# Optimization experiments

Measured on AMD Instinct MI355X. Metric: run time of the kernel, lower is better.

Reference implementation:

```python
import jax, jax.numpy as jnp
import numpy as np

N = 100000   # nodes
E = 1600000  # edges
IN = 32      # in_dim
D = 64       # embed_dim
G = 128      # num graphs
EPS = 1e-5   # BatchNorm eps


def setup_inputs() -> dict:
    key = jax.random.key(0)
    ks = jax.random.split(key, 12)
    s_in = 1.0 / np.sqrt(IN)
    s_d = 1.0 / np.sqrt(D)
    return {
        "x": jax.random.normal(ks[0], (N, IN), jnp.float32),
        "edge_index": jax.random.randint(ks[1], (2, E), 0, N),
        "batch": jnp.sort(jax.random.randint(ks[2], (N,), 0, G)),
        "W_embed": jax.random.normal(ks[3], (IN, D), jnp.float32) * s_in,
        "W1": jax.random.normal(ks[4], (D, D), jnp.float32) * s_d,
        "b1": jnp.zeros((D,), jnp.float32),
        "g1": jnp.ones((D,), jnp.float32),
        "bt1": jnp.zeros((D,), jnp.float32),
        "W2": jax.random.normal(ks[5], (D, D), jnp.float32) * s_d,
        "b2": jnp.zeros((D,), jnp.float32),
        "g2": jnp.ones((D,), jnp.float32),
        "bt2": jnp.zeros((D,), jnp.float32),
    }


def reference(x, edge_index, batch, W_embed, W1, b1, g1, bt1, W2, b2, g2, bt2):
    src, dst = edge_index[0], edge_index[1]
    # GCN symmetric norm with self loops: deg = in-degree + 1 (self loop)
    deg = jnp.zeros((N,), x.dtype).at[dst].add(1.0) + 1.0
    dis = jax.lax.rsqrt(deg)                      # deg^{-1/2}, [N]
    enorm = dis[src] * dis[dst]                   # per-edge norm, [E]
    self_norm = dis * dis                         # self-loop norm, [N]

    def gcn_bn(h, W, b, g, bt, relu):
        hw = h @ W                                # linear first (GCNConv)
        msg = hw[src] * enorm[:, None]            # [E, D] gather + scale
        agg = jax.ops.segment_sum(msg, dst, num_segments=N)
        agg = agg + hw * self_norm[:, None] + b   # self loops + bias
        # BatchNorm1d (training mode: batch stats, biased var)
        mu = agg.mean(axis=0)
        var = agg.var(axis=0)
        hn = (agg - mu) * jax.lax.rsqrt(var + EPS) * g + bt
        return jnp.maximum(hn, 0.0) if relu else hn

    h = x @ W_embed                               # node_embed (Linear, no bias)
    h = gcn_bn(h, W1, b1, g1, bt1, relu=True)     # ReLU only between layers
    h = gcn_bn(h, W2, b2, g2, bt2, relu=False)
    h_pool = jax.ops.segment_sum(h, batch, num_segments=G)  # global_add_pool
    return (h, h_pool)
```

## Files before the change

kernel.cpp:

```cpp
#include <hip/hip_runtime.h>

#define NN 100000
#define NE 1600000
#define IN_DIM 32
#define DD 64
#define NG 128
#define BN_EPS 1e-5f
#define AGG_BLOCKS 2048

typedef unsigned short ushort_t;
typedef unsigned int uint_t;

__device__ __forceinline__ ushort_t f2bf(float f) {
    uint_t u = __float_as_uint(f);
    u = (u + 0x7FFFu + ((u >> 16) & 1u)) >> 16;
    return (ushort_t)u;
}
__device__ __forceinline__ uint_t pack2(float a, float b) {
    return (uint_t)f2bf(a) | ((uint_t)f2bf(b) << 16);
}
__device__ __forceinline__ float bflo(uint_t u) { return __uint_as_float(u << 16); }
__device__ __forceinline__ float bfhi(uint_t u) { return __uint_as_float(u & 0xFFFF0000u); }

__global__ void init_k(int* __restrict__ ints, long n_ints, float* __restrict__ pool,
                       float* __restrict__ sums) {
    long i = (long)blockIdx.x * blockDim.x + threadIdx.x;
    if (i < n_ints) ints[i] = 0;
    if (i < (long)NG * DD) pool[i] = 0.f;
    if (i < 256) sums[i] = 0.f;
}

__global__ void deg_rank(const int* __restrict__ dst, int* __restrict__ cnt,
                         int* __restrict__ rank) {
    int e = blockIdx.x * blockDim.x + threadIdx.x;
    if (e < NE) rank[e] = atomicAdd(&cnt[dst[e]], 1);
}

__global__ __launch_bounds__(256) void alloc_k(const int* __restrict__ cnt,
                                               int* __restrict__ start,
                                               int* __restrict__ cursor,
                                               float* __restrict__ dis) {
    __shared__ int ls[256];
    __shared__ int base_s;
    int t = threadIdx.x;
    long n = (long)blockIdx.x * 256 + t;
    int v = (n < NN) ? cnt[n] : 0;
    ls[t] = v;
    __syncthreads();
    for (int off = 1; off < 256; off <<= 1) {
        int y = (t >= off) ? ls[t - off] : 0;
        __syncthreads();
        ls[t] += y;
        __syncthreads();
    }
    if (t == 0) base_s = atomicAdd(cursor, ls[255]);
    __syncthreads();
    if (n < NN) {
        start[n] = base_s + ls[t] - v;
        dis[n] = rsqrtf((float)v + 1.0f);
    }
}

__global__ void fill_edges(const int* __restrict__ src, const int* __restrict__ dstp,
                           const int* __restrict__ rank, const float* __restrict__ dis,
                           const int* __restrict__ start, uint_t* __restrict__ ep) {
    int e = blockIdx.x * blockDim.x + threadIdx.x;
    if (e >= NE) return;
    int s = src[e], t = dstp[e];
    float nm = dis[s] * dis[t];
    uint_t nb = (__float_as_uint(nm) + 0x8000u) >> 16;
    ep[start[t] + rank[e]] = (uint_t)s | ((nb & 0x7FFFu) << 17);
}

__global__ __launch_bounds__(256) void mm1_k(const float* __restrict__ x,
                                             const float* __restrict__ We,
                                             const float* __restrict__ W1,
                                             ushort_t* __restrict__ hwb) {
    __shared__ float W1s[DD * DD];
    __shared__ float Ws[IN_DIM * DD];
    int t = threadIdx.x;
    for (int i = t; i < DD * DD; i += 256) W1s[i] = W1[i];
    __syncthreads();
    for (int idx = t; idx < IN_DIM * DD; idx += 256) {
        int i = idx >> 6, j = idx & 63;
        float s = 0.f;
#pragma unroll
        for (int k = 0; k < DD; ++k) s += We[i * DD + k] * W1s[k * DD + j];
        Ws[idx] = s;
    }
    __syncthreads();
    long n = (long)blockIdx.x * 256 + t;
    if (n >= NN) return;
    float acc[DD];
#pragma unroll
    for (int d = 0; d < DD; ++d) acc[d] = 0.f;
    const float4* xr = (const float4*)(x + n * IN_DIM);
#pragma unroll
    for (int k4 = 0; k4 < IN_DIM / 4; ++k4) {
        float4 xv = xr[k4];
        const float* xp = (const float*)&xv;
#pragma unroll
        for (int kk = 0; kk < 4; ++kk) {
            float v = xp[kk];
            const float4* w4 = (const float4*)&Ws[(k4 * 4 + kk) * DD];
#pragma unroll
            for (int d4 = 0; d4 < DD / 4; ++d4) {
                float4 wv = w4[d4];
                acc[4 * d4 + 0] += v * wv.x;
                acc[4 * d4 + 1] += v * wv.y;
                acc[4 * d4 + 2] += v * wv.z;
                acc[4 * d4 + 3] += v * wv.w;
            }
        }
    }
    uint4* o = (uint4*)(hwb + n * DD);
#pragma unroll
    for (int d8 = 0; d8 < DD / 8; ++d8) {
        uint4 pk;
        pk.x = pack2(acc[8 * d8 + 0], acc[8 * d8 + 1]);
        pk.y = pack2(acc[8 * d8 + 2], acc[8 * d8 + 3]);
        pk.z = pack2(acc[8 * d8 + 4], acc[8 * d8 + 5]);
        pk.w = pack2(acc[8 * d8 + 6], acc[8 * d8 + 7]);
        o[d8] = pk;
    }
}

__global__ __launch_bounds__(256) void mm2_bn_k(const ushort_t* __restrict__ aggb,
                                                const float* __restrict__ sums,
                                                const float* __restrict__ g,
                                                const float* __restrict__ bt,
                                                const float* __restrict__ W,
                                                ushort_t* __restrict__ hwb) {
    __shared__ float Ws[DD * DD];
    __shared__ float mu_s[DD], sc_s[DD], bt_s[DD];
    int t = threadIdx.x;
    for (int i = t; i < DD * DD; i += 256) Ws[i] = W[i];
    if (t < DD) {
        const float inv_n = 1.0f / (float)NN;
        float mu = sums[t] * inv_n;
        float var = sums[64 + t] * inv_n - mu * mu;
        mu_s[t] = mu;
        sc_s[t] = g[t] * rsqrtf(var + BN_EPS);
        bt_s[t] = bt[t];
    }
    __syncthreads();
    long n = (long)blockIdx.x * 256 + t;
    if (n >= NN) return;
    float acc[DD];
#pragma unroll
    for (int d = 0; d < DD; ++d) acc[d] = 0.f;
    const uint4* ar = (const uint4*)(aggb + n * DD);
#pragma unroll
    for (int k8 = 0; k8 < DD / 8; ++k8) {
        uint4 av = ar[k8];
        float hv[8];
        hv[0] = bflo(av.x); hv[1] = bfhi(av.x);
        hv[2] = bflo(av.y); hv[3] = bfhi(av.y);
        hv[4] = bflo(av.z); hv[5] = bfhi(av.z);
        hv[6] = bflo(av.w); hv[7] = bfhi(av.w);
#pragma unroll
        for (int kk = 0; kk < 8; ++kk) {
            int k = k8 * 8 + kk;
            float h = fmaxf((hv[kk] - mu_s[k]) * sc_s[k] + bt_s[k], 0.f);
            const float4* w4 = (const float4*)&Ws[k * DD];
#pragma unroll
            for (int d4 = 0; d4 < DD / 4; ++d4) {
                float4 wv = w4[d4];
                acc[4 * d4 + 0] += h * wv.x;
                acc[4 * d4 + 1] += h * wv.y;
                acc[4 * d4 + 2] += h * wv.z;
                acc[4 * d4 + 3] += h * wv.w;
            }
        }
    }
    uint4* o = (uint4*)(hwb + n * DD);
#pragma unroll
    for (int d8 = 0; d8 < DD / 8; ++d8) {
        uint4 pk;
        pk.x = pack2(acc[8 * d8 + 0], acc[8 * d8 + 1]);
        pk.y = pack2(acc[8 * d8 + 2], acc[8 * d8 + 3]);
        pk.z = pack2(acc[8 * d8 + 4], acc[8 * d8 + 5]);
        pk.w = pack2(acc[8 * d8 + 6], acc[8 * d8 + 7]);
        o[d8] = pk;
    }
}

template <int WAGG_BF16>
__global__ __launch_bounds__(256) void gcn_agg(const ushort_t* __restrict__ hwb,
                                               const float* __restrict__ dis,
                                               const int* __restrict__ cnt,
                                               const int* __restrict__ start,
                                               const uint_t* __restrict__ ep,
                                               const float* __restrict__ bias,
                                               void* __restrict__ aggv,
                                               float* __restrict__ sums) {
    int t = threadIdx.x;
    int w = t >> 6;
    int lane = t & 63;
    int j = lane >> 3;
    int c = lane & 7;
    float selfmask = (j == 0) ? 1.f : 0.f;

    __shared__ float ls[4][128];
    for (int k = t; k < 512; k += 256) ((float*)ls)[k] = 0.f;
    __syncthreads();

    float bs[8];
#pragma unroll
    for (int k = 0; k < 8; ++k) bs[k] = bias[8 * c + k];

    for (long n = (long)blockIdx.x * 4 + w; n < NN; n += (long)gridDim.x * 4) {
        int rs = start[n];
        int ce = cnt[n];
        float sn = dis[n];
        float sq = sn * sn;

        uint4 sv = ((const uint4*)(hwb + (long)n * DD))[c];
        float acc[8];
        acc[0] = selfmask * (bflo(sv.x) * sq + bs[0]);
        acc[1] = selfmask * (bfhi(sv.x) * sq + bs[1]);
        acc[2] = selfmask * (bflo(sv.y) * sq + bs[2]);
        acc[3] = selfmask * (bfhi(sv.y) * sq + bs[3]);
        acc[4] = selfmask * (bflo(sv.z) * sq + bs[4]);
        acc[5] = selfmask * (bfhi(sv.z) * sq + bs[5]);
        acc[6] = selfmask * (bflo(sv.w) * sq + bs[6]);
        acc[7] = selfmask * (bfhi(sv.w) * sq + bs[7]);

        for (int i = 0; i < ce; i += 32) {
            int i0 = i + j, i1 = i + 8 + j, i2 = i + 16 + j, i3 = i + 24 + j;
            uint_t u0 = (i0 < ce) ? ep[rs + i0] : 0u;
            uint_t u1 = (i1 < ce) ? ep[rs + i1] : 0u;
            uint_t u2 = (i2 < ce) ? ep[rs + i2] : 0u;
            uint_t u3 = (i3 < ce) ? ep[rs + i3] : 0u;
            uint4 q0 = ((const uint4*)(hwb + (long)(u0 & 0x1FFFF) * DD))[c];
            uint4 q1 = ((const uint4*)(hwb + (long)(u1 & 0x1FFFF) * DD))[c];
            uint4 q2 = ((const uint4*)(hwb + (long)(u2 & 0x1FFFF) * DD))[c];
            uint4 q3 = ((const uint4*)(hwb + (long)(u3 & 0x1FFFF) * DD))[c];
            float n0 = __uint_as_float((u0 >> 17) << 16);
            float n1 = __uint_as_float((u1 >> 17) << 16);
            float n2 = __uint_as_float((u2 >> 17) << 16);
            float n3 = __uint_as_float((u3 >> 17) << 16);
            acc[0] += bflo(q0.x) * n0; acc[1] += bfhi(q0.x) * n0;
            acc[2] += bflo(q0.y) * n0; acc[3] += bfhi(q0.y) * n0;
            acc[4] += bflo(q0.z) * n0; acc[5] += bfhi(q0.z) * n0;
            acc[6] += bflo(q0.w) * n0; acc[7] += bfhi(q0.w) * n0;
            acc[0] += bflo(q1.x) * n1; acc[1] += bfhi(q1.x) * n1;
            acc[2] += bflo(q1.y) * n1; acc[3] += bfhi(q1.y) * n1;
            acc[4] += bflo(q1.z) * n1; acc[5] += bfhi(q1.z) * n1;
            acc[6] += bflo(q1.w) * n1; acc[7] += bfhi(q1.w) * n1;
            acc[0] += bflo(q2.x) * n2; acc[1] += bfhi(q2.x) * n2;
            acc[2] += bflo(q2.y) * n2; acc[3] += bfhi(q2.y) * n2;
            acc[4] += bflo(q2.z) * n2; acc[5] += bfhi(q2.z) * n2;
            acc[6] += bflo(q2.w) * n2; acc[7] += bfhi(q2.w) * n2;
            acc[0] += bflo(q3.x) * n3; acc[1] += bfhi(q3.x) * n3;
            acc[2] += bflo(q3.y) * n3; acc[3] += bfhi(q3.y) * n3;
            acc[4] += bflo(q3.z) * n3; acc[5] += bfhi(q3.z) * n3;
            acc[6] += bflo(q3.w) * n3; acc[7] += bfhi(q3.w) * n3;
        }

#pragma unroll
        for (int m = 8; m < 64; m <<= 1) {
#pragma unroll
            for (int k = 0; k < 8; ++k) acc[k] += __shfl_xor(acc[k], m, 64);
        }

        if (j == 0) {
            if (WAGG_BF16) {
                uint4 pk;
                pk.x = pack2(acc[0], acc[1]);
                pk.y = pack2(acc[2], acc[3]);
                pk.z = pack2(acc[4], acc[5]);
                pk.w = pack2(acc[6], acc[7]);
                ((uint4*)((ushort_t*)aggv + (long)n * DD))[c] = pk;
            } else {
                float4* op = (float4*)((float*)aggv + (long)n * DD + 8 * c);
                op[0] = make_float4(acc[0], acc[1], acc[2], acc[3]);
                op[1] = make_float4(acc[4], acc[5], acc[6], acc[7]);
            }
#pragma unroll
            for (int k = 0; k < 8; ++k) {
                ls[w][8 * c + k] += acc[k];
                ls[w][64 + 8 * c + k] += acc[k] * acc[k];
            }
        }
    }

    __syncthreads();
    if (t < 128) {
        float a = ls[0][t] + ls[1][t] + ls[2][t] + ls[3][t];
        atomicAdd(&sums[t], a);
    }
}

__global__ __launch_bounds__(256) void bn_pool(const float* __restrict__ agg,
                                               const float* __restrict__ sums,
                                               const float* __restrict__ g,
                                               const float* __restrict__ bt,
                                               const int* __restrict__ batch,
                                               float* __restrict__ out,
                                               float* __restrict__ pool) {
    int t = threadIdx.x;
    int d = t & 63, rq = t >> 6;
    const float inv_n = 1.0f / (float)NN;
    float mu = sums[d] * inv_n;
    float var = sums[64 + d] * inv_n - mu * mu;
    float sc = g[d] * rsqrtf(var + BN_EPS);
    float bd = bt[d];
    long base = (long)blockIdx.x * 256;
    float acc = 0.f;
    int cur = -1;
    for (int i = 0; i < 64; ++i) {
        long r = base + rq + 4 * i;
        if (r >= NN) break;
        int b = batch[r];
        float v = (agg[r * DD + d] - mu) * sc + bd;
        out[r * DD + d] = v;
        if (b != cur) {
            if (cur >= 0) atomicAdd(&pool[(long)cur * DD + d], acc);
            acc = 0.f;
            cur = b;
        }
        acc += v;
    }
    if (cur >= 0) atomicAdd(&pool[(long)cur * DD + d], acc);
}

extern "C" void kernel_launch(void* const* d_in, const int* in_sizes, int n_in,
                              void* d_out, int out_size, void* d_ws, size_t ws_size,
                              hipStream_t stream) {
    const float* x = (const float*)d_in[0];
    const int* ei = (const int*)d_in[1];
    const int* batch = (const int*)d_in[2];
    const float* W_embed = (const float*)d_in[3];
    const float* W1 = (const float*)d_in[4];
    const float* b1 = (const float*)d_in[5];
    const float* g1 = (const float*)d_in[6];
    const float* bt1 = (const float*)d_in[7];
    const float* W2 = (const float*)d_in[8];
    const float* b2 = (const float*)d_in[9];
    const float* g2 = (const float*)d_in[10];
    const float* bt2 = (const float*)d_in[11];

    const int* src = ei;
    const int* dst = ei + NE;

    float* out = (float*)d_out;
    float* pool = out + (long)NN * DD;

    const long ND = (long)NN * DD;

    char* w = (char*)d_ws;
    int* cnt = (int*)w;           w += sizeof(int) * NN;
    int* cursor = (int*)w;        w += sizeof(int) * 4;
    int* start = (int*)w;         w += sizeof(int) * NN;
    float* dis = (float*)w;       w += sizeof(float) * NN;
    float* sums1 = (float*)w;     w += sizeof(float) * 128;
    float* sums2 = (float*)w;     w += sizeof(float) * 128;
    int* rank = (int*)w;          w += sizeof(int) * NE;
    uint_t* ep = (uint_t*)w;      w += sizeof(uint_t) * NE;
    ushort_t* hwb = (ushort_t*)w; w += sizeof(ushort_t) * ND;
    ushort_t* agg1b = (ushort_t*)w; w += sizeof(ushort_t) * ND;
    float* aggbuf = (float*)w;

    dim3 blk(256);
    const int nbN = (NN + 255) / 256;
    const int nbE = (NE + 255) / 256;
    const long n_ints = (long)NN + 4;

    init_k<<<dim3((int)((n_ints + 255) / 256)), blk, 0, stream>>>(cnt, n_ints, pool, sums1);
    deg_rank<<<dim3(nbE), blk, 0, stream>>>(dst, cnt, rank);
    alloc_k<<<dim3(nbN), blk, 0, stream>>>(cnt, start, cursor, dis);
    fill_edges<<<dim3(nbE), blk, 0, stream>>>(src, dst, rank, dis, start, ep);

    mm1_k<<<dim3(nbN), blk, 0, stream>>>(x, W_embed, W1, hwb);

    gcn_agg<1><<<dim3(AGG_BLOCKS), blk, 0, stream>>>(hwb, dis, cnt, start, ep, b1,
                                                     (void*)agg1b, sums1);

    mm2_bn_k<<<dim3(nbN), blk, 0, stream>>>(agg1b, sums1, g1, bt1, W2, hwb);

    gcn_agg<0><<<dim3(AGG_BLOCKS), blk, 0, stream>>>(hwb, dis, cnt, start, ep, b2,
                                                     (void*)aggbuf, sums2);

    bn_pool<<<dim3(nbN), blk, 0, stream>>>(aggbuf, sums2, g2, bt2, batch, out, pool);
}
```

Baseline: 422.7 us.

## Use bf16 MFMA for the fused BatchNorm+ReLU second-layer matmul

Replaces the scalar per-thread 64x64 FMA loop in the BN+ReLU+matmul kernel with MFMA 16x16x32 bf16 instructions. W2 is converted to bf16 and swizzled into shared memory in fragment order, and activations are normalized and packed into bf16 A fragments. This cuts per-thread FMA and register cost. In exchange it adds bf16 rounding of the normalized activations and weights, and uses scattered 2-byte output stores.

```diff
diff --git a/kernel.cpp b/kernel.cpp
--- a/kernel.cpp
+++ b/kernel.cpp
@@ -10,6 +10,8 @@
 
 typedef unsigned short ushort_t;
 typedef unsigned int uint_t;
+typedef __attribute__((ext_vector_type(8))) short bf16x8;
+typedef __attribute__((ext_vector_type(4))) float f32x4;
 
 __device__ __forceinline__ ushort_t f2bf(float f) {
     uint_t u = __float_as_uint(f);
@@ -125,16 +127,15 @@
     }
 }
 
-__global__ __launch_bounds__(256) void mm2_bn_k(const ushort_t* __restrict__ aggb,
-                                                const float* __restrict__ sums,
-                                                const float* __restrict__ g,
-                                                const float* __restrict__ bt,
-                                                const float* __restrict__ W,
-                                                ushort_t* __restrict__ hwb) {
-    __shared__ float Ws[DD * DD];
+__global__ __launch_bounds__(256) void mm2_bn_mfma(const ushort_t* __restrict__ aggb,
+                                                   const float* __restrict__ sums,
+                                                   const float* __restrict__ g,
+                                                   const float* __restrict__ bt,
+                                                   const float* __restrict__ W,
+                                                   ushort_t* __restrict__ hwb) {
+    __shared__ ushort_t Wf[2 * 4 * 64 * 8];
     __shared__ float mu_s[DD], sc_s[DD], bt_s[DD];
     int t = threadIdx.x;
-    for (int i = t; i < DD * DD; i += 256) Ws[i] = W[i];
     if (t < DD) {
         const float inv_n = 1.0f / (float)NN;
         float mu = sums[t] * inv_n;
@@ -143,45 +144,74 @@
         sc_s[t] = g[t] * rsqrtf(var + BN_EPS);
         bt_s[t] = bt[t];
     }
-    __syncthreads();
-    long n = (long)blockIdx.x * 256 + t;
-    if (n >= NN) return;
-    float acc[DD];
-#pragma unroll
-    for (int d = 0; d < DD; ++d) acc[d] = 0.f;
-    const uint4* ar = (const uint4*)(aggb + n * DD);
-#pragma unroll
-    for (int k8 = 0; k8 < DD / 8; ++k8) {
-        uint4 av = ar[k8];
-        float hv[8];
-        hv[0] = bflo(av.x); hv[1] = bfhi(av.x);
-        hv[2] = bflo(av.y); hv[3] = bfhi(av.y);
-        hv[4] = bflo(av.z); hv[5] = bfhi(av.z);
-        hv[6] = bflo(av.w); hv[7] = bfhi(av.w);
-#pragma unroll
-        for (int kk = 0; kk < 8; ++kk) {
-            int k = k8 * 8 + kk;
-            float h = fmaxf((hv[kk] - mu_s[k]) * sc_s[k] + bt_s[k], 0.f);
-            const float4* w4 = (const float4*)&Ws[k * DD];
-#pragma unroll
-            for (int d4 = 0; d4 < DD / 4; ++d4) {
-                float4 wv = w4[d4];
-                acc[4 * d4 + 0] += h * wv.x;
-                acc[4 * d4 + 1] += h * wv.y;
-                acc[4 * d4 + 2] += h * wv.z;
-                acc[4 * d4 + 3] += h * wv.w;
+    for (int e = t; e < 4096; e += 256) {
+        int ks = e >> 11;
+        int c = (e >> 9) & 3;
+        int l = (e >> 3) & 63;
+        int j = e & 7;
+        int k = ks * 32 + ((l >> 4) << 3) + j;
+        int col = c * 16 + (l & 15);
+        Wf[e] = f2bf(W[k * DD + col]);
+    }
+    __syncthreads();
+
+    int w = t >> 6, l = t & 63;
+    int lr = l & 15, lk = l >> 4;
+
+#pragma unroll
+    for (int gi = 0; gi < 4; ++gi) {
+        long rowbase = (long)blockIdx.x * 256 + w * 64 + gi * 16;
+        long r = rowbase + lr;
+
+        bf16x8 afrag[2];
+#pragma unroll
+        for (int ks = 0; ks < 2; ++ks) {
+            int k0 = ks * 32 + (lk << 3);
+            uint4 av = (r < NN) ? *(const uint4*)(aggb + r * DD + k0)
+                                : make_uint4(0, 0, 0, 0);
+            float4 muA = *(const float4*)&mu_s[k0];
+            float4 muB = *(const float4*)&mu_s[k0 + 4];
+            float4 scA = *(const float4*)&sc_s[k0];
+            float4 scB = *(const float4*)&sc_s[k0 + 4];
+            float4 btA = *(const float4*)&bt_s[k0];
+            float4 btB = *(const float4*)&bt_s[k0 + 4];
+            float h0 = fmaxf((bflo(av.x) - muA.x) * scA.x + btA.x, 0.f);
+            float h1 = fmaxf((bfhi(av.x) - muA.y) * scA.y + btA.y, 0.f);
+            float h2 = fmaxf((bflo(av.y) - muA.z) * scA.z + btA.z, 0.f);
+            float h3 = fmaxf((bfhi(av.y) - muA.w) * scA.w + btA.w, 0.f);
+            float h4 = fmaxf((bflo(av.z) - muB.x) * scB.x + btB.x, 0.f);
+            float h5 = fmaxf((bfhi(av.z) - muB.y) * scB.y + btB.y, 0.f);
+            float h6 = fmaxf((bflo(av.w) - muB.z) * scB.z + btB.z, 0.f);
+            float h7 = fmaxf((bfhi(av.w) - muB.w) * scB.w + btB.w, 0.f);
+            bf16x8 fr;
+            fr[0] = (short)f2bf(h0); fr[1] = (short)f2bf(h1);
+            fr[2] = (short)f2bf(h2); fr[3] = (short)f2bf(h3);
+            fr[4] = (short)f2bf(h4); fr[5] = (short)f2bf(h5);
+            fr[6] = (short)f2bf(h6); fr[7] = (short)f2bf(h7);
+            afrag[ks] = fr;
+        }
+
+        f32x4 acc[4];
+#pragma unroll
+        for (int c = 0; c < 4; ++c) acc[c] = (f32x4){0.f, 0.f, 0.f, 0.f};
+#pragma unroll
+        for (int c = 0; c < 4; ++c) {
+#pragma unroll
+            for (int ks = 0; ks < 2; ++ks) {
+                bf16x8 bfr = *(bf16x8*)&Wf[((ks * 4 + c) << 9) + (l << 3)];
+                acc[c] = __builtin_amdgcn_mfma_f32_16x16x32_bf16(afrag[ks], bfr, acc[c],
+                                                                 0, 0, 0);
             }
         }
-    }
-    uint4* o = (uint4*)(hwb + n * DD);
-#pragma unroll
-    for (int d8 = 0; d8 < DD / 8; ++d8) {
-        uint4 pk;
-        pk.x = pack2(acc[8 * d8 + 0], acc[8 * d8 + 1]);
-        pk.y = pack2(acc[8 * d8 + 2], acc[8 * d8 + 3]);
-        pk.z = pack2(acc[8 * d8 + 4], acc[8 * d8 + 5]);
-        pk.w = pack2(acc[8 * d8 + 6], acc[8 * d8 + 7]);
-        o[d8] = pk;
+
+#pragma unroll
+        for (int c = 0; c < 4; ++c) {
+#pragma unroll
+            for (int rr = 0; rr < 4; ++rr) {
+                long orow = rowbase + lk * 4 + rr;
+                if (orow < NN) hwb[orow * DD + c * 16 + lr] = f2bf(acc[c][rr]);
+            }
+        }
     }
 }
 
@@ -377,7 +407,7 @@
     gcn_agg<1><<<dim3(AGG_BLOCKS), blk, 0, stream>>>(hwb, dis, cnt, start, ep, b1,
                                                      (void*)agg1b, sums1);
 
-    mm2_bn_k<<<dim3(nbN), blk, 0, stream>>>(agg1b, sums1, g1, bt1, W2, hwb);
+    mm2_bn_mfma<<<dim3(nbN), blk, 0, stream>>>(agg1b, sums1, g1, bt1, W2, hwb);
 
     gcn_agg<0><<<dim3(AGG_BLOCKS), blk, 0, stream>>>(hwb, dis, cnt, start, ep, b2,
                                                      (void*)aggbuf, sums2);
```

Result: faster. 401.2 us (median of 2 runs) (-5.1%).
